# Kernel tuning notes

Hardware: AMD Instinct MI355X
Metric: run time of the kernel (lower is better)

## Reference

```python
import jax, jax.numpy as jnp
import numpy as np

GH, GW, GC = 256, 256, 8  # learned warp grid shape
TWO_PI = 2.0 * np.pi


def setup_inputs() -> dict:
    key = jax.random.key(0)
    k1, k2 = jax.random.split(key)
    image = jax.random.normal(k1, (16, 512, 512, 4), dtype=jnp.float32)
    weight = jax.random.normal(k2, (GH, GW, GC), dtype=jnp.float32)
    return {"image": image, "weight": weight}


def reference(image, weight):
    # typ != 'xyz': map interleaved (x, y) channel pairs to angular coords in [0, 1)
    # image[..., 0::2] -> x coords, image[..., 1::2] -> y coords; each [B,H,W,2]
    C = np.pi - jnp.arctan2(image[..., 1::2], -image[..., 0::2])
    C = C / TWO_PI
    shape_mult = jnp.asarray([GH, GW], dtype=jnp.float32)  # broadcasts over [B,H,W,2]
    C = C * (shape_mult - 1.0)
    C = jnp.clip(C, 0.0, shape_mult - 2.0)

    # bilinear interpolation into weight grid [GH, GW, GC]
    w = C - jnp.floor(C)                      # fractional parts [B,H,W,2]
    w0, w1 = w[..., 0:1], w[..., 1:2]         # [B,H,W,1] each
    idx = C.astype(jnp.int32)
    i0, j0 = idx[..., 0], idx[..., 1]          # [B,H,W]

    def corner(di, dj):
        return weight[i0 + di, j0 + dj]        # gather -> [B,H,W,GC]

    res = (corner(0, 0) * (1.0 - w0) * (1.0 - w1)
           + corner(1, 0) * w0 * (1.0 - w1)
           + corner(0, 1) * (1.0 - w0) * w1
           + corner(1, 1) * w0 * w1)

    W = res * 0.0005                           # [B,H,W,GC]
    return jnp.concatenate([W, image], axis=3)  # [B,H,W,GC+4]
```

## Files before the change

kernel.cpp:

```cpp
#include <hip/hip_runtime.h>
#include <math.h>


#define GH 256
#define GW 256

__device__ __forceinline__ float4 f4_mad(float4 a, float s, float4 acc) {
    acc.x = fmaf(a.x, s, acc.x);
    acc.y = fmaf(a.y, s, acc.y);
    acc.z = fmaf(a.z, s, acc.z);
    acc.w = fmaf(a.w, s, acc.w);
    return acc;
}

__global__ __launch_bounds__(256) void warp_kernel(
    const float4* __restrict__ img,
    const float4* __restrict__ wq,
    float4*       __restrict__ out,
    int npix)
{
    __shared__ float4 lds_g[2048];
    __shared__ int    lds_a[256];

    const int t    = threadIdx.x;
    const int base = blockIdx.x * 256;

    const float PI    = 3.14159265358979323846f;
    const float SCALE = 255.0f / (2.0f * PI);
    const float OUT_SCALE = 0.0005f;

    if (base + 256 > npix) {
        int p = base + t;
        if (p >= npix) return;
        float4 px = img[p];
        float c0 = (PI - atan2f(px.y, -px.x)) * SCALE;
        float c1 = (PI - atan2f(px.w, -px.z)) * SCALE;
        c0 = fminf(fmaxf(c0, 0.0f), 254.0f);
        c1 = fminf(fmaxf(c1, 0.0f), 254.0f);
        int i0 = (int)c0, j0 = (int)c1;
        float w0 = c0 - (float)i0, w1 = c1 - (float)j0;
        float f00 = (1.0f - w0) * (1.0f - w1), f10 = w0 * (1.0f - w1);
        float f01 = (1.0f - w0) * w1,          f11 = w0 * w1;
        int b00 = (i0 * GW + j0) * 2, b10 = b00 + GW * 2;
        float4 ra = make_float4(0,0,0,0), rb = make_float4(0,0,0,0);
        ra = f4_mad(wq[b00],   f00, ra); rb = f4_mad(wq[b00+1], f00, rb);
        ra = f4_mad(wq[b00+2], f01, ra); rb = f4_mad(wq[b00+3], f01, rb);
        ra = f4_mad(wq[b10],   f10, ra); rb = f4_mad(wq[b10+1], f10, rb);
        ra = f4_mad(wq[b10+2], f11, ra); rb = f4_mad(wq[b10+3], f11, rb);
        ra.x*=OUT_SCALE; ra.y*=OUT_SCALE; ra.z*=OUT_SCALE; ra.w*=OUT_SCALE;
        rb.x*=OUT_SCALE; rb.y*=OUT_SCALE; rb.z*=OUT_SCALE; rb.w*=OUT_SCALE;
        int ob = p * 3;
        out[ob] = ra; out[ob+1] = rb; out[ob+2] = px;
        return;
    }

    int p = base + t;
    float4 px = img[p];
    float c0 = (PI - atan2f(px.y, -px.x)) * SCALE;
    float c1 = (PI - atan2f(px.w, -px.z)) * SCALE;
    c0 = fminf(fmaxf(c0, 0.0f), 254.0f);
    c1 = fminf(fmaxf(c1, 0.0f), 254.0f);
    int i0 = (int)c0, j0 = (int)c1;
    float w0 = c0 - (float)i0, w1 = c1 - (float)j0;
    lds_a[t] = (i0 * GW + j0) * 2;
    __syncthreads();

    #pragma unroll
    for (int k = 0; k < 8; k++) {
        int g  = t + (k << 8);
        int pp = g >> 3;
        int hc = g & 7;
        int h  = hc >> 2;
        int c  = hc & 3;
        int addr = lds_a[pp] + h * (GW * 2) + c;
        float4 v = wq[addr];
        lds_g[pp * 8 + (hc ^ (pp & 7))] = v;
    }
    __syncthreads();

    float4 q[8];
    #pragma unroll
    for (int c2 = 0; c2 < 8; c2++)
        q[c2] = lds_g[t * 8 + (c2 ^ (t & 7))];

    float f00 = (1.0f - w0) * (1.0f - w1);
    float f10 = w0 * (1.0f - w1);
    float f01 = (1.0f - w0) * w1;
    float f11 = w0 * w1;

    float4 ra = make_float4(0,0,0,0), rb = make_float4(0,0,0,0);
    ra = f4_mad(q[0], f00, ra); rb = f4_mad(q[1], f00, rb);
    ra = f4_mad(q[2], f01, ra); rb = f4_mad(q[3], f01, rb);
    ra = f4_mad(q[4], f10, ra); rb = f4_mad(q[5], f10, rb);
    ra = f4_mad(q[6], f11, ra); rb = f4_mad(q[7], f11, rb);
    ra.x*=OUT_SCALE; ra.y*=OUT_SCALE; ra.z*=OUT_SCALE; ra.w*=OUT_SCALE;
    rb.x*=OUT_SCALE; rb.y*=OUT_SCALE; rb.z*=OUT_SCALE; rb.w*=OUT_SCALE;

    __syncthreads();
    lds_g[t * 3 + 0] = ra;
    lds_g[t * 3 + 1] = rb;
    lds_g[t * 3 + 2] = px;
    __syncthreads();

    int ob = base * 3;
    out[ob + t]       = lds_g[t];
    out[ob + 256 + t] = lds_g[256 + t];
    out[ob + 512 + t] = lds_g[512 + t];
}

extern "C" void kernel_launch(void* const* d_in, const int* in_sizes, int n_in,
                              void* d_out, int out_size, void* d_ws, size_t ws_size,
                              hipStream_t stream) {
    const float4* img = (const float4*)d_in[0];
    const float4* wq  = (const float4*)d_in[1];
    float4*       out = (float4*)d_out;

    int npix = in_sizes[0] / 4;
    int block = 256;
    int grid = (npix + block - 1) / block;

    warp_kernel<<<grid, block, 0, stream>>>(img, wq, out, npix);
}
```

Before: 282.4 us.

## Replace block-wide LDS gather staging with per-wave shuffle reductions

The cooperative corner gather moves from block-level LDS staging to wave-local work. Each lane fetches one float4 of a pixel's eight corner values, scales it by its bilinear factor, and sums across lanes with xor shuffles. Results go into a per-wave LDS stage, which cuts shared memory use and drops two block barriers. The cost is extra shuffle instructions and idle lanes during the stage writes. The one remaining __syncthreads could in principle be relaxed, since each wave only reads its own stage region.

```diff
diff --git a/kernel.cpp b/kernel.cpp
--- a/kernel.cpp
+++ b/kernel.cpp
@@ -2,7 +2,6 @@
 #include <math.h>
 
 
-#define GH 256
 #define GW 256
 
 __device__ __forceinline__ float4 f4_mad(float4 a, float s, float4 acc) {
@@ -19,14 +18,15 @@
     float4*       __restrict__ out,
     int npix)
 {
-    __shared__ float4 lds_g[2048];
-    __shared__ int    lds_a[256];
+    __shared__ float4 stage[4 * 192];
 
     const int t    = threadIdx.x;
+    const int lane = t & 63;
+    const int wv   = t >> 6;
     const int base = blockIdx.x * 256;
 
-    const float PI    = 3.14159265358979323846f;
-    const float SCALE = 255.0f / (2.0f * PI);
+    const float PI        = 3.14159265358979323846f;
+    const float SCALE     = 255.0f / (2.0f * PI);
     const float OUT_SCALE = 0.0005f;
 
     if (base + 256 > npix) {
@@ -54,58 +54,51 @@
         return;
     }
 
-    int p = base + t;
-    float4 px = img[p];
+    const int pw = base + wv * 64;
+    float4 px = img[pw + lane];
+
     float c0 = (PI - atan2f(px.y, -px.x)) * SCALE;
     float c1 = (PI - atan2f(px.w, -px.z)) * SCALE;
     c0 = fminf(fmaxf(c0, 0.0f), 254.0f);
     c1 = fminf(fmaxf(c1, 0.0f), 254.0f);
     int i0 = (int)c0, j0 = (int)c1;
     float w0 = c0 - (float)i0, w1 = c1 - (float)j0;
-    lds_a[t] = (i0 * GW + j0) * 2;
+    int abase = i0 * (GW * 2) + j0 * 2;
+
+    float4* mystage = stage + wv * 192;
+    mystage[lane * 3 + 2] = px;
+
+    const int hc  = lane & 7;
+    const int sub = lane >> 3;
+    #pragma unroll
+    for (int k = 0; k < 8; k++) {
+        int   p8  = (k << 3) + sub;
+        int   ab  = __shfl(abase, p8, 64);
+        float pw0 = __shfl(w0,    p8, 64);
+        float pw1 = __shfl(w1,    p8, 64);
+        float f0  = (hc & 4) ? pw0 : (1.0f - pw0);
+        float f1  = (hc & 2) ? pw1 : (1.0f - pw1);
+        float fac = f0 * f1 * OUT_SCALE;
+        int   off = ((hc & 4) ? (GW * 2) : 0) + ((hc & 2) ? 2 : 0) + (hc & 1);
+
+        float4 v = wq[ab + off];
+        float rx = v.x * fac, ry = v.y * fac, rz = v.z * fac, rw = v.w * fac;
+
+        rx += __shfl_xor(rx, 2, 64); ry += __shfl_xor(ry, 2, 64);
+        rz += __shfl_xor(rz, 2, 64); rw += __shfl_xor(rw, 2, 64);
+        rx += __shfl_xor(rx, 4, 64); ry += __shfl_xor(ry, 4, 64);
+        rz += __shfl_xor(rz, 4, 64); rw += __shfl_xor(rw, 4, 64);
+
+        if (hc < 2)
+            mystage[p8 * 3 + hc] = make_float4(rx, ry, rz, rw);
+    }
+
     __syncthreads();
 
-    #pragma unroll
-    for (int k = 0; k < 8; k++) {
-        int g  = t + (k << 8);
-        int pp = g >> 3;
-        int hc = g & 7;
-        int h  = hc >> 2;
-        int c  = hc & 3;
-        int addr = lds_a[pp] + h * (GW * 2) + c;
-        float4 v = wq[addr];
-        lds_g[pp * 8 + (hc ^ (pp & 7))] = v;
-    }
-    __syncthreads();
-
-    float4 q[8];
-    #pragma unroll
-    for (int c2 = 0; c2 < 8; c2++)
-        q[c2] = lds_g[t * 8 + (c2 ^ (t & 7))];
-
-    float f00 = (1.0f - w0) * (1.0f - w1);
-    float f10 = w0 * (1.0f - w1);
-    float f01 = (1.0f - w0) * w1;
-    float f11 = w0 * w1;
-
-    float4 ra = make_float4(0,0,0,0), rb = make_float4(0,0,0,0);
-    ra = f4_mad(q[0], f00, ra); rb = f4_mad(q[1], f00, rb);
-    ra = f4_mad(q[2], f01, ra); rb = f4_mad(q[3], f01, rb);
-    ra = f4_mad(q[4], f10, ra); rb = f4_mad(q[5], f10, rb);
-    ra = f4_mad(q[6], f11, ra); rb = f4_mad(q[7], f11, rb);
-    ra.x*=OUT_SCALE; ra.y*=OUT_SCALE; ra.z*=OUT_SCALE; ra.w*=OUT_SCALE;
-    rb.x*=OUT_SCALE; rb.y*=OUT_SCALE; rb.z*=OUT_SCALE; rb.w*=OUT_SCALE;
-
-    __syncthreads();
-    lds_g[t * 3 + 0] = ra;
-    lds_g[t * 3 + 1] = rb;
-    lds_g[t * 3 + 2] = px;
-    __syncthreads();
-
-    int ob = base * 3;
-    out[ob + t]       = lds_g[t];
-    out[ob + 256 + t] = lds_g[256 + t];
-    out[ob + 512 + t] = lds_g[512 + t];
+    int ob = base * 3 + wv * 192;
+    out[ob + lane]       = mystage[lane];
+    out[ob + 64 + lane]  = mystage[64 + lane];
+    out[ob + 128 + lane] = mystage[128 + lane];
 }
 
 extern "C" void kernel_launch(void* const* d_in, const int* in_sizes, int n_in,
```

Result: slower. 289.0 us (+2.4%).
